# Optimization experiments

Hardware: AMD Instinct MI355X
Metric: run time of the kernel (lower is better)

## Reference

```python
import jax, jax.numpy as jnp
import numpy as np

N = 4608      # total nodes (48 graphs x 96 nodes)
B = 48
NPG = 96
D = 512       # vec_dim
XD = 16       # x_dim
E = N * 32    # GAT edges
L = 6         # GAT layers


def _w(k, shape, fan_in):
    return jax.random.normal(k, shape, jnp.float32) * (1.0 / np.sqrt(fan_in))


def setup_inputs() -> dict:
    key = jax.random.key(0)
    ks = jax.random.split(key, 24)
    x = jax.random.normal(ks[0], (N, XD), jnp.float32)
    xyz = jax.random.normal(ks[1], (N, 3), jnp.float32)
    edge_index = jax.random.randint(ks[2], (2, E), 0, N, dtype=jnp.int32)
    ptr = (jnp.arange(B + 1) * NPG).astype(jnp.int32)
    # complete graph with replacement per segment (torch.combinations order: i<=j)
    i, j = np.triu_indices(NPG)
    offs = (np.arange(B) * NPG)[:, None]
    cloud_edge_index = jnp.asarray(
        np.stack([(i[None, :] + offs).reshape(-1), (j[None, :] + offs).reshape(-1)]),
        jnp.int32)
    return {
        'x': x, 'edge_index': edge_index, 'ptr': ptr, 'xyz': xyz,
        'cloud_edge_index': cloud_edge_index,
        'x_proj_w': _w(ks[3], (XD, D), XD), 'x_proj_b': jnp.zeros((D,), jnp.float32),
        'gat_wl': _w(ks[4], (L, D, D), D), 'gat_bl': jnp.zeros((L, D), jnp.float32),
        'gat_wr': _w(ks[5], (L, D, D), D), 'gat_br': jnp.zeros((L, D), jnp.float32),
        'gat_att': _w(ks[6], (L, D), D), 'gat_bias': jnp.zeros((L, D), jnp.float32),
        'gat_ln_g': jnp.ones((L - 1, D), jnp.float32), 'gat_ln_b': jnp.zeros((L - 1, D), jnp.float32),
        'cg_xyz_w': _w(ks[7], (3, D), 3),
        'cg_bn_g': jnp.ones((D,), jnp.float32), 'cg_bn_b': jnp.zeros((D,), jnp.float32),
        'cg_lin1_w': _w(ks[8], (D, D), D), 'cg_lin1_b': jnp.zeros((D,), jnp.float32),
        'cg_ln_g': jnp.ones((D,), jnp.float32), 'cg_ln_b': jnp.zeros((D,), jnp.float32),
        'lin_w': _w(ks[9], (D, D), D), 'lin_b': jnp.zeros((D,), jnp.float32),
        'bn_g': jnp.ones((D,), jnp.float32), 'bn_b': jnp.zeros((D,), jnp.float32),
    }


def _batchnorm(t, g, b):
    mu = t.mean(0)
    v = ((t - mu) ** 2).mean(0)
    return (t - mu) / jnp.sqrt(v + 1e-5) * g + b


def _forward(x, edge_index, cloud_edge_index, x_proj_w, x_proj_b, gat_wl, gat_bl,
             gat_wr, gat_br, gat_att, gat_bias, gat_ln_g, gat_ln_b, cg_xyz_w,
             cg_bn_g, cg_bn_b, cg_lin1_w, cg_lin1_b, cg_ln_g, cg_ln_b,
             lin_w, lin_b, bn_g, bn_b, xyz):
    n = x.shape[0]
    h = x @ x_proj_w + x_proj_b  # [N, D]
    # ---- GATv2 stack (heads=1, self-loops added, eval mode: no dropout) ----
    loops = jnp.arange(n, dtype=edge_index.dtype)
    ei = jnp.concatenate([edge_index, jnp.stack([loops, loops])], axis=1)
    src, dst = ei[0], ei[1]
    xg = h
    for l in range(L):
        xl = xg @ gat_wl[l] + gat_bl[l]
        xr = xg @ gat_wr[l] + gat_br[l]
        e = jax.nn.leaky_relu(xl[src] + xr[dst], 0.2) @ gat_att[l]  # [E+N]
        m = jax.ops.segment_max(e, dst, num_segments=n)
        ew = jnp.exp(e - m[dst])
        den = jax.ops.segment_sum(ew, dst, num_segments=n)
        alpha = ew / den[dst]
        out = jax.ops.segment_sum(alpha[:, None] * xl[src], dst, num_segments=n) + gat_bias[l]
        if l < L - 1:
            # PyG LayerNorm, mode='graph', batch=None: normalize over all elements
            mu = out.mean()
            sd = jnp.sqrt(((out - mu) ** 2).mean())
            out = (out - mu) / (sd + 1e-5) * gat_ln_g[l] + gat_ln_b[l]
            out = jax.nn.relu(out)
        xg = out
    # ---- CloudGraph (complete graph gather-compute-scatter) ----
    a, b = cloud_edge_index[0], cloud_edge_index[1]
    rx = h[a] - h[b]          # [Ec, D]
    rz = xyz[a] - xyz[b]      # [Ec, 3]
    sq = (rz ** 2).sum(-1)
    dist = jnp.where(sq > 0, jnp.sqrt(jnp.where(sq > 0, sq, 1.0)), 0.0)
    w = jnp.exp(-dist)[:, None]
    p1 = jax.ops.segment_sum(jax.nn.relu((w * rx) @ cg_lin1_w + cg_lin1_b), a, num_segments=n)
    mu1 = p1.mean(-1, keepdims=True)
    v1 = ((p1 - mu1) ** 2).mean(-1, keepdims=True)
    ln1 = (p1 - mu1) / jnp.sqrt(v1 + 1e-5) * cg_ln_g + cg_ln_b
    p2 = jax.ops.segment_sum(jax.nn.relu(rz @ cg_xyz_w), a, num_segments=n)
    xc = h + ln1 + _batchnorm(p2, cg_bn_g, cg_bn_b)
    # ---- fuse + final norm ----
    return _batchnorm((h + xg + xc) @ lin_w + lin_b, bn_g, bn_b)


def reference(x, edge_index, ptr, xyz, cloud_edge_index, x_proj_w, x_proj_b,
              gat_wl, gat_bl, gat_wr, gat_br, gat_att, gat_bias, gat_ln_g,
              gat_ln_b, cg_xyz_w, cg_bn_g, cg_bn_b, cg_lin1_w, cg_lin1_b,
              cg_ln_g, cg_ln_b, lin_w, lin_b, bn_g, bn_b):
    return _forward(x, edge_index, cloud_edge_index, x_proj_w, x_proj_b, gat_wl,
                    gat_bl, gat_wr, gat_br, gat_att, gat_bias, gat_ln_g,
                    gat_ln_b, cg_xyz_w, cg_bn_g, cg_bn_b, cg_lin1_w, cg_lin1_b,
                    cg_ln_g, cg_ln_b, lin_w, lin_b, bn_g, bn_b, xyz)
```

## Files before the change

### kernel.cpp

```cpp
#include <hip/hip_runtime.h>
#include <hip/hip_bf16.h>

#define NN 4608
#define BG 48
#define NPG 96
#define DD 512
#define XDIM 16
#define EREAL 147456
#define NLAYER 6
#define NK 262144
#define TRIU 4656

typedef __hip_bfloat16 bf16;
typedef short short8 __attribute__((ext_vector_type(8)));
typedef short shortx4 __attribute__((ext_vector_type(4)));
typedef float f32x4 __attribute__((ext_vector_type(4)));
typedef float f32x2 __attribute__((ext_vector_type(2)));

__device__ __forceinline__ float s2f(short s) {
  return __uint_as_float(((unsigned int)(unsigned short)s) << 16);
}
__device__ __forceinline__ short f2bs(float f) {
  bf16 h = __float2bfloat16(f);
  short s;
// ... 38 lines not shown
  bf16* dst = Wt + (size_t)z * NK;
  int c = threadIdx.x & 31;
  int r0 = threadIdx.x >> 5;
  int bx = blockIdx.x * 32, by = blockIdx.y * 32;
#pragma unroll
  for (int i = 0; i < 4; i++) {
    int r = r0 + i * 8;
    tile[r][c] = src[(size_t)(by + r) * 512 + bx + c];
  }
  __syncthreads();
#pragma unroll
  for (int i = 0; i < 4; i++) {
    int r = r0 + i * 8;
    dst[(size_t)(bx + r) * 512 + by + c] = __float2bfloat16(tile[c][r]);
  }
}

__global__ void k_xproj(const float* __restrict__ x, const float* __restrict__ w,
                        const float* __restrict__ b, const int* __restrict__ ei,
                        const float* __restrict__ xyz,
                        bf16* __restrict__ h_bf, int* __restrict__ counts,
                        float* __restrict__ ep) {
  int i = blockIdx.x * blockDim.x + threadIdx.x;
  if (i >= NN * DD) return;
  if (i < EREAL) atomicAdd(&counts[ei[EREAL + i]], 1);
  if (i < NN * NPG) {
    int n = i / NPG, e = i - n * NPG;
    int p = n % NPG;
    if (e < NPG - p) {
      int g = n / NPG;
      int slot = g * TRIU + p * NPG - (p * (p - 1)) / 2 + e;
      int j = n + e;
      float dx = xyz[n * 3] - xyz[j * 3];
      float dy = xyz[n * 3 + 1] - xyz[j * 3 + 1];
      float dz = xyz[n * 3 + 2] - xyz[j * 3 + 2];
      float sq = dx * dx + dy * dy + dz * dz;
      float dist = (sq > 0.f) ? sqrtf(sq) : 0.f;
      float4 v;
      v.x = dx; v.y = dy; v.z = dz; v.w = __expf(-dist);
      *(float4*)&ep[(size_t)slot * 4] = v;
    }
  }
  int n = i >> 9, d = i & 511;
  float acc = b[d];
#pragma unroll
  for (int k = 0; k < XDIM; k++) acc += x[n * XDIM + k] * w[k * DD + d];
  h_bf[i] = __float2bfloat16(acc);
}

__global__ void k_scan(const int* __restrict__ counts, int* offsets, int* cursor) {
  __shared__ int part[256];
  int t = threadIdx.x;
  int base = t * 18;
  int s = 0;
#pragma unroll
  for (int i = 0; i < 18; i++) s += counts[base + i];
  part[t] = s;
  __syncthreads();
  for (int off = 1; off < 256; off <<= 1) {
    int v = part[t];
    int u = (t >= off) ? part[t - off] : 0;
    __syncthreads();
    part[t] = v + u;
    __syncthreads();
  }
  int run = t ? part[t - 1] : 0;
#pragma unroll
  for (int i = 0; i < 18; i++) {
    offsets[base + i] = run;
    cursor[base + i] = run;
    run += counts[base + i];
  }
  if (t == 0) offsets[NN] = EREAL;
}
__global__ void k_scatter(const int* __restrict__ ei, int* cursor, int* ssrc) {
  int e = blockIdx.x * blockDim.x + threadIdx.x;
  if (e < EREAL) {
    int s = ei[e], d = ei[EREAL + e];
    int pos = atomicAdd(&cursor[d], 1);
    ssrc[pos] = s;
  }
}

__global__ __launch_bounds__(256) void k_ln(const bf16* __restrict__ in,
                                            bf16* __restrict__ out,
                                            const float* __restrict__ stats,
                                            const float* __restrict__ g,
                                            const float* __restrict__ b) {
  float s = 0.f, ss = 0.f;
#pragma unroll
  for (int i = 0; i < 16; i++) { s += stats[i]; ss += stats[16 + i]; }
  const float invM = 1.f / ((float)NN * (float)DD);
  float mu = s * invM;
  float var = ss * invM - mu * mu;
  float sd = sqrtf(fmaxf(var, 0.f));
  float inv = 1.f / (sd + 1e-5f);
  int i = blockIdx.x * 256 + threadIdx.x;
  int base = i * 8;
  int d0 = base & 511;
  short8 raw = *(const short8*)&in[base];
  short8 pk;
#pragma unroll
  for (int k = 0; k < 8; k++) {
    float t = fmaxf((s2f(raw[k]) - mu) * inv * g[d0 + k] + b[d0 + k], 0.f);
    pk[k] = f2bs(t);
  }
  *(short8*)&out[base] = pk;
}

__global__ __launch_bounds__(256) void k_gemm(
    const bf16* __restrict__ Abf,
    const bf16* __restrict__ B0, const bf16* __restrict__ B1,
    const float* __restrict__ bias0, const float* __restrict__ bias1,
    float* __restrict__ C0, float* __restrict__ C1,
    bf16* __restrict__ Cb0, bf16* __restrict__ Cb1,
    unsigned char* __restrict__ Cf8_0, unsigned char* __restrict__ Cf8_1,
    float* __restrict__ zptr, int zn,
    float* __restrict__ csum, float* __restrict__ csq, int nzl) {
  if (zptr && blockIdx.x == 0) {
    for (int i = threadIdx.x; i < zn; i += 256) zptr[i] = 0.f;
  }
  __shared__ __align__(16) bf16 As[2][128 * 64];
  __shared__ __align__(16) bf16 Bs[2][64 * 64];
  __shared__ float cs[64], cq[64];
  int cpx = gridDim.x >> 3;
  int wgid = (blockIdx.x & 7) * cpx + (blockIdx.x >> 3);
  int mi = wgid >> nzl;
  int r = wgid & ((1 << nzl) - 1);
  int z = r >> 3;
  int m0 = mi * 128, n0 = (r & 7) * 64;

  const bf16* B = z ? B1 : B0;
  const float* bias = z ? bias1 : bias0;
  float* C = z ? C1 : C0;
  bf16* Cb = z ? Cb1 : Cb0;
  unsigned char* Cf8 = z ? Cf8_1 : Cf8_0;
  int tid = threadIdx.x;
  int lane = tid & 63, wid = tid >> 6;
  int mh = (wid >> 1) * 64, nh = (wid & 1) * 32;
  int l15 = lane & 15, quad = lane >> 4;
  int lr8 = lane >> 3;
  int ls8 = lane & 7;
  int c16l = ls8 ^ (lr8 & 7);
  int swzr = (l15 & 7) * 8;

  if (csum && tid < 64) { cs[tid] = 0.f; cq[tid] = 0.f; }

  const bf16* aSrc = Abf + (size_t)(m0 + wid * 32 + lr8) * 512 + c16l * 8;
  const bf16* bSrc = B   + (size_t)(n0 + wid * 16 + lr8) * 512 + c16l * 8;

#define STAGE(bi, kt) do {                                              \
    gl16(aSrc + (kt) * 64,            &As[bi][(wid * 32     ) * 64]);   \
    gl16(aSrc + (kt) * 64 +  8 * 512, &As[bi][(wid * 32 +  8) * 64]);   \
    gl16(aSrc + (kt) * 64 + 16 * 512, &As[bi][(wid * 32 + 16) * 64]);   \
    gl16(aSrc + (kt) * 64 + 24 * 512, &As[bi][(wid * 32 + 24) * 64]);   \
    gl16(bSrc + (kt) * 64,            &Bs[bi][(wid * 16     ) * 64]);   \
    gl16(bSrc + (kt) * 64 +  8 * 512, &Bs[bi][(wid * 16 +  8) * 64]);   \
  } while (0)

  f32x4 acc[4][2];
#pragma unroll
  for (int mt = 0; mt < 4; mt++)
#pragma unroll
    for (int nt = 0; nt < 2; nt++) acc[mt][nt] = (f32x4)0.f;

  STAGE(0, 0);
  __syncthreads();

#pragma unroll
  for (int kt = 0; kt < 8; kt++) {
    const int cur = kt & 1;
    if (kt < 7) STAGE(cur ^ 1, kt + 1);
    short8 af[2][4], bfr[2][2];
#pragma unroll
    for (int kk = 0; kk < 2; kk++) {
#pragma unroll
      for (int mt = 0; mt < 4; mt++)
        af[kk][mt] = *(const short8*)&As[cur][(mh + mt * 16 + l15) * 64 +
                                             (((kk * 4 + quad) * 8) ^ swzr)];
#pragma unroll
      for (int nt = 0; nt < 2; nt++)
        bfr[kk][nt] = *(const short8*)&Bs[cur][(nh + nt * 16 + l15) * 64 +
                                              (((kk * 4 + quad) * 8) ^ swzr)];
    }
#pragma unroll
    for (int kk = 0; kk < 2; kk++)
#pragma unroll
      for (int mt = 0; mt < 4; mt++)
#pragma unroll
        for (int nt = 0; nt < 2; nt++)
          acc[mt][nt] = __builtin_amdgcn_mfma_f32_16x16x32_bf16(
              bfr[kk][nt], af[kk][mt], acc[mt][nt], 0, 0, 0);
    __syncthreads();
  }
#undef STAGE

  float colS[2][4] = {{0.f,0.f,0.f,0.f},{0.f,0.f,0.f,0.f}};
  float colQ[2][4] = {{0.f,0.f,0.f,0.f},{0.f,0.f,0.f,0.f}};
  float bv[2][4] = {{0.f,0.f,0.f,0.f},{0.f,0.f,0.f,0.f}};
#pragma unroll
  for (int nt = 0; nt < 2; nt++) {
    if (bias) {
      float4 b4 = *(const float4*)&bias[n0 + nh + nt * 16 + quad * 4];
      bv[nt][0] = b4.x; bv[nt][1] = b4.y; bv[nt][2] = b4.z; bv[nt][3] = b4.w;
    }
  }
#pragma unroll
  for (int mt = 0; mt < 4; mt++) {
    int row = m0 + mh + mt * 16 + l15;
#pragma unroll
    for (int nt = 0; nt < 2; nt++) {
      int col0 = n0 + nh + nt * 16 + quad * 4;
      float v[4];
#pragma unroll
      for (int r2 = 0; r2 < 4; r2++) {
        v[r2] = acc[mt][nt][r2] + bv[nt][r2];
        if (csum) { colS[nt][r2] += v[r2]; colQ[nt][r2] += v[r2] * v[r2]; }
      }
      if (C) {
        float4 o; o.x = v[0]; o.y = v[1]; o.z = v[2]; o.w = v[3];
        *(float4*)&C[(size_t)row * 512 + col0] = o;
      }
      if (Cb) {
        shortx4 o;
#pragma unroll
        for (int r2 = 0; r2 < 4; r2++) o[r2] = f2bs(v[r2]);
        *(shortx4*)&Cb[(size_t)row * 512 + col0] = o;
      }
      if (Cf8) {
        unsigned int u = __builtin_amdgcn_cvt_pk_fp8_f32(v[0], v[1], 0, false);
        u = __builtin_amdgcn_cvt_pk_fp8_f32(v[2], v[3], u, true);
        *(unsigned int*)&Cf8[(size_t)row * 512 + col0] = u;
      }
    }
  }
  if (csum) {
#pragma unroll
    for (int nt = 0; nt < 2; nt++)
#pragma unroll
      for (int r2 = 0; r2 < 4; r2++) {
        atomicAdd(&cs[nh + nt * 16 + quad * 4 + r2], colS[nt][r2]);
        atomicAdd(&cq[nh + nt * 16 + quad * 4 + r2], colQ[nt][r2]);
      }
    __syncthreads();
    if (tid < 64) {
      atomicAdd(&csum[n0 + tid], cs[tid]);
      atomicAdd(&csq[n0 + tid], cq[tid]);
    }
  }
}

__global__ __launch_bounds__(256) void k_gat_edge(const unsigned char* __restrict__ xl8,
                                                  const bf16* __restrict__ xr,
                                                  const float* __restrict__ att,
                                                  const float* __restrict__ bias,
                                                  const int* __restrict__ offs,
                                                  const int* __restrict__ ssrc,
                                                  bf16* __restrict__ out,
                                                  float* __restrict__ statsOut) {
  __shared__ float redS[4], redSS[4];
  int wave = (blockIdx.x * blockDim.x + threadIdx.x) >> 6;
  int lane = threadIdx.x & 63;
  int wid = threadIdx.x >> 6;
  if (wave < NN) {
    int n = wave;
    int base = lane * 8;
    float xrv[8], attv[8], acc[8];
    short8 xr8 = *(const short8*)&xr[(size_t)n * 512 + base];
#pragma unroll
    for (int k = 0; k < 8; k++) {
      xrv[k] = s2f(xr8[k]);
      attv[k] = att[base + k];
    }
    float m0, lsum;
    {
      uint2 q = *(const uint2*)&xl8[(size_t)n * 512 + base];
      float xs[8];
      f8x4(q.x, xs);
      f8x4(q.y, xs + 4);
      float sc0 = 0.f;
#pragma unroll
      for (int k = 0; k < 8; k++) {
        acc[k] = xs[k];
        float t = xs[k] + xrv[k];
        t = (t > 0.f) ? t : 0.2f * t;
        sc0 += attv[k] * t;
      }
#pragma unroll
      for (int off = 32; off >= 1; off >>= 1) sc0 += __shfl_xor(sc0, off, 64);
      m0 = sc0;
      lsum = 1.f;
    }
    int e0 = offs[n], e1 = offs[n + 1];
    int e = e0;
    for (; e + 3 < e1; e += 4) {
      int s0 = ssrc[e], s1 = ssrc[e + 1], s2 = ssrc[e + 2], s3 = ssrc[e + 3];
      uint2 q0 = *(const uint2*)&xl8[(size_t)s0 * 512 + base];
      uint2 q1 = *(const uint2*)&xl8[(size_t)s1 * 512 + base];
      uint2 q2 = *(const uint2*)&xl8[(size_t)s2 * 512 + base];
      uint2 q3 = *(const uint2*)&xl8[(size_t)s3 * 512 + base];
      float x0[8], x1[8], x2[8], x3[8];
      f8x4(q0.x, x0); f8x4(q0.y, x0 + 4);
      f8x4(q1.x, x1); f8x4(q1.y, x1 + 4);
      f8x4(q2.x, x2); f8x4(q2.y, x2 + 4);
      f8x4(q3.x, x3); f8x4(q3.y, x3 + 4);
      float c0 = 0.f, c1 = 0.f, c2 = 0.f, c3 = 0.f;
#pragma unroll
      for (int k = 0; k < 8; k++) {
        float t0 = x0[k] + xrv[k]; t0 = (t0 > 0.f) ? t0 : 0.2f * t0; c0 += attv[k] * t0;
        float t1 = x1[k] + xrv[k]; t1 = (t1 > 0.f) ? t1 : 0.2f * t1; c1 += attv[k] * t1;
        float t2 = x2[k] + xrv[k]; t2 = (t2 > 0.f) ? t2 : 0.2f * t2; c2 += attv[k] * t2;
        float t3 = x3[k] + xrv[k]; t3 = (t3 > 0.f) ? t3 : 0.2f * t3; c3 += attv[k] * t3;
      }
#pragma unroll
      for (int off = 32; off >= 1; off >>= 1) {
        c0 += __shfl_xor(c0, off, 64);
        c1 += __shfl_xor(c1, off, 64);
        c2 += __shfl_xor(c2, off, 64);
        c3 += __shfl_xor(c3, off, 64);
      }
      float p0 = __expf(c0 - m0), p1 = __expf(c1 - m0);
      float p2 = __expf(c2 - m0), p3 = __expf(c3 - m0);
      lsum += p0 + p1 + p2 + p3;
#pragma unroll
      for (int k = 0; k < 8; k++)
        acc[k] += p0 * x0[k] + p1 * x1[k] + p2 * x2[k] + p3 * x3[k];
    }
    for (; e < e1; ++e) {
      int s0 = ssrc[e];
      uint2 q = *(const uint2*)&xl8[(size_t)s0 * 512 + base];
      float x0[8];
      f8x4(q.x, x0);
      f8x4(q.y, x0 + 4);
      float sc0 = 0.f;
#pragma unroll
      for (int k = 0; k < 8; k++) {
        float t0 = x0[k] + xrv[k];
        t0 = (t0 > 0.f) ? t0 : 0.2f * t0;
        sc0 += attv[k] * t0;
      }
#pragma unroll
      for (int off = 32; off >= 1; off >>= 1) sc0 += __shfl_xor(sc0, off, 64);
      float p0 = __expf(sc0 - m0);
      lsum += p0;
#pragma unroll
      for (int k = 0; k < 8; k++) acc[k] += p0 * x0[k];
    }
    float inv = 1.f / lsum;
    float o[8];
    float s = 0.f, ss = 0.f;
    short8 o8;
#pragma unroll
    for (int k = 0; k < 8; k++) {
      o[k] = acc[k] * inv + bias[base + k];
      s += o[k];
      ss += o[k] * o[k];
      o8[k] = f2bs(o[k]);
    }
    *(short8*)&out[(size_t)n * 512 + base] = o8;
    if (statsOut) {
#pragma unroll
      for (int off = 32; off >= 1; off >>= 1) {
        s += __shfl_xor(s, off, 64);
        ss += __shfl_xor(ss, off, 64);
      }
      if (lane == 0) { redS[wid] = s; redSS[wid] = ss; }
    }
  }
  if (statsOut) {
    __syncthreads();
    if (threadIdx.x == 0) {
      float a = redS[0] + redS[1] + redS[2] + redS[3];
      float b = redSS[0] + redSS[1] + redSS[2] + redSS[3];
      int slot = blockIdx.x & 15;
      atomicAdd(&statsOut[slot], a);
      atomicAdd(&statsOut[16 + slot], b);
    }
  }
}

__global__ __launch_bounds__(256) void k_cloud(const bf16* __restrict__ g1,
                                               const float* __restrict__ ep,
                                               const float* __restrict__ lin1b,
                                               const float* __restrict__ w3,
                                               float* __restrict__ p1,
                                               float* __restrict__ p2) {
  int w = (blockIdx.x * blockDim.x + threadIdx.x) >> 6;
  int lane = threadIdx.x & 63;
  if (w >= NN) return;
  int qh = w & 1;
  int pi = w >> 1;
  int g = pi / 48, pp = pi % 48;
  int d0 = qh * 256 + lane * 4;
  float4 bb4 = *(const float4*)&lin1b[d0];
  float4 w04 = *(const float4*)&w3[d0];
  float4 w14 = *(const float4*)&w3[512 + d0];
  float4 w24 = *(const float4*)&w3[1024 + d0];
  float bb[4] = {bb4.x, bb4.y, bb4.z, bb4.w};
  float w0[4] = {w04.x, w04.y, w04.z, w04.w};
  float w1[4] = {w14.x, w14.y, w14.z, w14.w};
  float w2[4] = {w24.x, w24.y, w24.z, w24.w};

#pragma unroll
  for (int half = 0; half < 2; half++) {
    int p = half ? (NPG - 1 - pp) : pp;
    int n = g * NPG + p;
    int cnt = NPG - p;
    int slot0 = g * TRIU + p * NPG - (p * (p - 1)) / 2;
    const bf16* grow = &g1[(size_t)n * 512 + d0];
    float gi[4];
    { uint2 q = *(const uint2*)grow; bf4(q, gi); }
    float a1[4] = {0.f,0.f,0.f,0.f}, a2[4] = {0.f,0.f,0.f,0.f};
    float b1[4] = {0.f,0.f,0.f,0.f}, b2[4] = {0.f,0.f,0.f,0.f};
    int e = 0;
    for (; e + 3 < cnt; e += 4) {
      int sb = __builtin_amdgcn_readfirstlane(slot0 + e);
      float4 pa = *(const float4*)&ep[(size_t)sb * 4];
      float4 pb = *(const float4*)&ep[(size_t)(sb + 1) * 4];
      float4 pc = *(const float4*)&ep[(size_t)(sb + 2) * 4];
      float4 pd = *(const float4*)&ep[(size_t)(sb + 3) * 4];
      uint2 qa = *(const uint2*)&grow[(size_t)e * 512];
      uint2 qb = *(const uint2*)&grow[(size_t)(e + 1) * 512];
      uint2 qc = *(const uint2*)&grow[(size_t)(e + 2) * 512];
      uint2 qd = *(const uint2*)&grow[(size_t)(e + 3) * 512];
      float xa[4], xb[4], xc[4], xd[4];
      bf4(qa, xa); bf4(qb, xb); bf4(qc, xc); bf4(qd, xd);
      float t;
#pragma unroll
      for (int k = 0; k < 4; k++) {
        t = fmaf(pa.w, gi[k] - xa[k], bb[k]); a1[k] += fmaxf(t, 0.f);
        t = fmaf(pb.w, gi[k] - xb[k], bb[k]); b1[k] += fmaxf(t, 0.f);
        t = fmaf(pc.w, gi[k] - xc[k], bb[k]); a1[k] += fmaxf(t, 0.f);
        t = fmaf(pd.w, gi[k] - xd[k], bb[k]); b1[k] += fmaxf(t, 0.f);
        t = pa.x * w0[k] + pa.y * w1[k] + pa.z * w2[k]; a2[k] += fmaxf(t, 0.f);
        t = pb.x * w0[k] + pb.y * w1[k] + pb.z * w2[k]; b2[k] += fmaxf(t, 0.f);
        t = pc.x * w0[k] + pc.y * w1[k] + pc.z * w2[k]; a2[k] += fmaxf(t, 0.f);
        t = pd.x * w0[k] + pd.y * w1[k] + pd.z * w2[k]; b2[k] += fmaxf(t, 0.f);
      }
    }
    for (; e < cnt; ++e) {
      float4 pa = *(const float4*)&ep[(size_t)(slot0 + e) * 4];
      uint2 qa = *(const uint2*)&grow[(size_t)e * 512];
      float xa[4];
      bf4(qa, xa);
      float t;
#pragma unroll
      for (int k = 0; k < 4; k++) {
        t = fmaf(pa.w, gi[k] - xa[k], bb[k]); a1[k] += fmaxf(t, 0.f);
        t = pa.x * w0[k] + pa.y * w1[k] + pa.z * w2[k]; a2[k] += fmaxf(t, 0.f);
      }
    }
    float4 o1, o2;
    o1.x = a1[0] + b1[0]; o1.y = a1[1] + b1[1];
    o1.z = a1[2] + b1[2]; o1.w = a1[3] + b1[3];
    o2.x = a2[0] + b2[0]; o2.y = a2[1] + b2[1];
    o2.z = a2[2] + b2[2]; o2.w = a2[3] + b2[3];
    *(float4*)&p1[(size_t)n * 512 + d0] = o1;
    *(float4*)&p2[(size_t)n * 512 + d0] = o2;
  }
}

__global__ __launch_bounds__(256) void k_cloud_epi(
    const float* __restrict__ p1, const float* __restrict__ p2,
    const bf16* __restrict__ h_bf, const bf16* __restrict__ xg_bf,
    const float* __restrict__ colsum, const float* __restrict__ colsq,
    const float* __restrict__ lng, const float* __restrict__ lnb,
    const float* __restrict__ bng, const float* __restrict__ bnb,
    bf16* __restrict__ s_bf, float* __restrict__ zptr) {
  if (blockIdx.x == 0) {
    for (int i = threadIdx.x; i < 1024; i += 256) zptr[i] = 0.f;
  }
  int wave = (blockIdx.x * blockDim.x + threadIdx.x) >> 6;
  int lane = threadIdx.x & 63;
  if (wave >= NN) return;
  int n = wave;
  size_t rb = (size_t)n * 512 + lane * 8;
  int base = lane * 8;
  float v[8];
  float s = 0.f;
#pragma unroll
  for (int k = 0; k < 8; k++) {
    v[k] = p1[rb + k];
    s += v[k];
  }
#pragma unroll
  for (int off = 32; off >= 1; off >>= 1) s += __shfl_xor(s, off, 64);
  float mu = s * (1.f / 512.f);
  float ss = 0.f;
#pragma unroll
  for (int k = 0; k < 8; k++) {
    float t = v[k] - mu;
    ss += t * t;
  }
#pragma unroll
  for (int off = 32; off >= 1; off >>= 1) ss += __shfl_xor(ss, off, 64);
  float inv = 1.f / sqrtf(ss * (1.f / 512.f) + 1e-5f);
  short8 hb = *(const short8*)&h_bf[rb];
  short8 xb = *(const short8*)&xg_bf[rb];
  short8 o8;
#pragma unroll
  for (int k = 0; k < 8; k++) {
    int d = base + k;
    float ln1 = (v[k] - mu) * inv * lng[d] + lnb[d];
    float cmu = colsum[d] * (1.f / NN);
    float cvar = colsq[d] * (1.f / NN) - cmu * cmu;
    float cinv = 1.f / sqrtf(fmaxf(cvar, 0.f) + 1e-5f);
    float bnv = (p2[rb + k] - cmu) * cinv * bng[d] + bnb[d];
    float out = 2.f * s2f(hb[k]) + s2f(xb[k]) + ln1 + bnv;
    o8[k] = f2bs(out);
  }
  *(short8*)&s_bf[rb] = o8;
}

__global__ void k_col_reduce(const float* __restrict__ x, float* colsum, float* colsq) {
  int r0 = blockIdx.x * 32;
  int c0 = threadIdx.x;
  float s0 = 0.f, q0 = 0.f, s1 = 0.f, q1 = 0.f;
  for (int r = r0; r < r0 + 32; ++r) {
    float v = x[(size_t)r * 512 + c0];
    s0 += v;
    q0 += v * v;
    float w = x[(size_t)r * 512 + c0 + 256];
    s1 += w;
    q1 += w * w;
  }
  atomicAdd(&colsum[c0], s0);
  atomicAdd(&colsq[c0], q0);
  atomicAdd(&colsum[c0 + 256], s1);
  atomicAdd(&colsq[c0 + 256], q1);
}
__global__ void k_bn_out(const float* __restrict__ y, const float* __restrict__ colsum,
                         const float* __restrict__ colsq, const float* __restrict__ g,
                         const float* __restrict__ b, float* __restrict__ out) {
  int i = blockIdx.x * blockDim.x + threadIdx.x;
  if (i >= NN * DD) return;
  int d = i & 511;
  float mu = colsum[d] * (1.f / NN);
  float var = colsq[d] * (1.f / NN) - mu * mu;
  float inv = 1.f / sqrtf(fmaxf(var, 0.f) + 1e-5f);
  out[i] = (y[i] - mu) * inv * g[d] + b[d];
}

extern "C" void kernel_launch(void* const* d_in, const int* in_sizes, int n_in,
                              void* d_out, int out_size, void* d_ws, size_t ws_size,
                              hipStream_t stream) {
  const float* x = (const float*)d_in[0];
  const int* ei = (const int*)d_in[1];
  const float* xyz = (const float*)d_in[3];
  const float* x_proj_w = (const float*)d_in[5];
  const float* x_proj_b = (const float*)d_in[6];
  const float* gat_wl = (const float*)d_in[7];
  const float* gat_bl = (const float*)d_in[8];
  const float* gat_wr = (const float*)d_in[9];
  const float* gat_br = (const float*)d_in[10];
  const float* gat_att = (const float*)d_in[11];
  const float* gat_bias = (const float*)d_in[12];
  const float* gat_ln_g = (const float*)d_in[13];
  const float* gat_ln_b = (const float*)d_in[14];
  const float* cg_xyz_w = (const float*)d_in[15];
  const float* cg_bn_g = (const float*)d_in[16];
  const float* cg_bn_b = (const float*)d_in[17];
  const float* cg_lin1_w = (const float*)d_in[18];
  const float* cg_lin1_b = (const float*)d_in[19];
  const float* cg_ln_g = (const float*)d_in[20];
  const float* cg_ln_b = (const float*)d_in[21];
  const float* lin_w = (const float*)d_in[22];
  const float* lin_b = (const float*)d_in[23];
  const float* bn_g = (const float*)d_in[24];
  const float* bn_b = (const float*)d_in[25];

  const size_t ND = (size_t)NN * DD;
  char* w = (char*)d_ws;
  float* p1 = (float*)w;       w += ND * 4;
  float* p2 = (float*)w;       w += ND * 4;
  bf16* h_bf = (bf16*)w;       w += ND * 2;
  bf16* xg_bf = (bf16*)w;      w += ND * 2;
  bf16* g1_bf = (bf16*)w;      w += ND * 2;
  bf16* xr_bf = (bf16*)w;      w += ND * 2;
  unsigned char* xl_f8 = (unsigned char*)w; w += ND;
  bf16* Wt = (bf16*)w;         w += (size_t)14 * NK * 2;
  float* eparam = (float*)w;   w += (size_t)BG * TRIU * 16;
  int* counts = (int*)w;       w += NN * 4;
  int* offs = (int*)w;         w += (NN + 4) * 4;
  int* cursor = (int*)w;       w += NN * 4;
  int* ssrc = (int*)w;         w += EREAL * 4;
  float* statsAll = (float*)w; w += 5 * 32 * 4;
  float* colsum = (float*)w;   w += 512 * 4;
  float* colsq = (float*)w;    w += 512 * 4;
  float* colsum2 = (float*)w;  w += 512 * 4;
  float* colsq2 = (float*)w;   w += 512 * 4;
  float* y = p1;
  bf16* s_bf = h_bf;
  bf16* aln_bf = g1_bf;

  const int TPB = 256;
  const int ND_BLK = (int)((ND + TPB - 1) / TPB);

  k_wt<<<dim3(16, 16, 14), TPB, 0, stream>>>(gat_wl, gat_wr, cg_lin1_w, lin_w, Wt,
                                             counts, statsAll);
  k_xproj<<<ND_BLK, TPB, 0, stream>>>(x, x_proj_w, x_proj_b, ei, xyz, h_bf,
                                      counts, eparam);
  k_scan<<<1, 256, 0, stream>>>(counts, offs, cursor);
  k_scatter<<<(EREAL + TPB - 1) / TPB, TPB, 0, stream>>>(ei, cursor, ssrc);

  for (int l = 0; l < NLAYER; l++) {
    const bf16* A;
    if (l == 0) {
      A = h_bf;
    } else {
      k_ln<<<(int)(ND / 8 / TPB), TPB, 0, stream>>>(
          xg_bf, aln_bf, statsAll + 32 * (l - 1),
          gat_ln_g + (size_t)(l - 1) * DD, gat_ln_b + (size_t)(l - 1) * DD);
      A = aln_bf;
    }
    k_gemm<<<576, TPB, 0, stream>>>(
        A, Wt + (size_t)l * NK, Wt + (size_t)(6 + l) * NK,
        gat_bl + l * DD, gat_br + l * DD, nullptr, nullptr, nullptr, xr_bf,
        xl_f8, nullptr, nullptr, 0, nullptr, nullptr, 4);
    float* sOut = (l < NLAYER - 1) ? statsAll + 32 * l : nullptr;
    k_gat_edge<<<NN / 4, TPB, 0, stream>>>(xl_f8, xr_bf, gat_att + l * DD,
                                           gat_bias + l * DD, offs, ssrc,
                                           xg_bf, sOut);
  }

  k_gemm<<<288, TPB, 0, stream>>>(
      h_bf, Wt + (size_t)12 * NK, Wt + (size_t)12 * NK, nullptr, nullptr,
      nullptr, nullptr, g1_bf, g1_bf, nullptr, nullptr,
      colsum, 1024, nullptr, nullptr, 3);
  k_cloud<<<NN / 4, TPB, 0, stream>>>(g1_bf, eparam, cg_lin1_b, cg_xyz_w, p1, p2);
  k_col_reduce<<<144, 256, 0, stream>>>(p2, colsum, colsq);
  k_cloud_epi<<<NN / 4, TPB, 0, stream>>>(p1, p2, h_bf, xg_bf, colsum, colsq,
                                          cg_ln_g, cg_ln_b, cg_bn_g, cg_bn_b,
                                          s_bf, colsum2);

  k_gemm<<<288, TPB, 0, stream>>>(
      s_bf, Wt + (size_t)13 * NK, Wt + (size_t)13 * NK, lin_b, lin_b,
      y, y, nullptr, nullptr, nullptr, nullptr,
      nullptr, 0, colsum2, colsq2, 3);
  k_bn_out<<<ND_BLK, TPB, 0, stream>>>(y, colsum2, colsq2, bn_g, bn_b,
                                       (float*)d_out);
}
```

Baseline: 542.6 us.

## Merge cloud-branch kernels into GAT layer launches to fill the GPU

The cloud lin1 GEMM becomes extra blocks of the layer-0 GAT projection GEMM. The cloud pairwise aggregation becomes extra blocks of the layer-0 edge kernel, split into half-waves per node pair. The p2 column reduction runs as extra blocks of the layer-1 LayerNorm kernel, which now also writes in place into xg. This removes three launches and lets the independent cloud branch fill idle CUs during small GAT kernels, at the cost of heterogeneous blocks and possible load imbalance.

Result: faster. 522.7 us (-3.7%).

```diff
diff --git a/kernel.cpp b/kernel.cpp
--- a/kernel.cpp
+++ b/kernel.cpp
@@ -144,11 +144,29 @@
   }
 }
 
-__global__ __launch_bounds__(256) void k_ln(const bf16* __restrict__ in,
-                                            bf16* __restrict__ out,
+__global__ __launch_bounds__(256) void k_ln(bf16* __restrict__ xg,
                                             const float* __restrict__ stats,
                                             const float* __restrict__ g,
-                                            const float* __restrict__ b) {
+                                            const float* __restrict__ b,
+                                            const float* __restrict__ p2,
+                                            float* __restrict__ colsum,
+                                            float* __restrict__ colsq) {
+  if ((int)blockIdx.x >= 1152) {
+    int r0 = (blockIdx.x - 1152) * 32;
+    int c0 = threadIdx.x;
+    float s0 = 0.f, q0 = 0.f, s1 = 0.f, q1 = 0.f;
+    for (int r = r0; r < r0 + 32; ++r) {
+      float v = p2[(size_t)r * 512 + c0];
+      s0 += v; q0 += v * v;
+      float w = p2[(size_t)r * 512 + c0 + 256];
+      s1 += w; q1 += w * w;
+    }
+    atomicAdd(&colsum[c0], s0);
+    atomicAdd(&colsq[c0], q0);
+    atomicAdd(&colsum[c0 + 256], s1);
+    atomicAdd(&colsq[c0 + 256], q1);
+    return;
+  }
   float s = 0.f, ss = 0.f;
 #pragma unroll
   for (int i = 0; i < 16; i++) { s += stats[i]; ss += stats[16 + i]; }
@@ -160,30 +178,146 @@
   int i = blockIdx.x * 256 + threadIdx.x;
   int base = i * 8;
   int d0 = base & 511;
-  short8 raw = *(const short8*)&in[base];
+  short8 raw = *(const short8*)&xg[base];
   short8 pk;
 #pragma unroll
   for (int k = 0; k < 8; k++) {
     float t = fmaxf((s2f(raw[k]) - mu) * inv * g[d0 + k] + b[d0 + k], 0.f);
     pk[k] = f2bs(t);
   }
-  *(short8*)&out[base] = pk;
+  *(short8*)&xg[base] = pk;
+}
+
+__device__ __forceinline__ void gemm_tile(
+    const bf16* __restrict__ Abf, const bf16* __restrict__ B,
+    const float* __restrict__ bias,
+    float* __restrict__ C, bf16* __restrict__ Cb, unsigned char* __restrict__ Cf8,
+    float* __restrict__ csum, float* __restrict__ csq,
+    int m0, int n0, bf16* As, bf16* Bs, float* cs, float* cq) {
+  int tid = threadIdx.x;
+  int lane = tid & 63, wid = tid >> 6;
+  int mh = (wid >> 1) * 64, nh = (wid & 1) * 32;
+  int l15 = lane & 15, quad = lane >> 4;
+  int lr8 = lane >> 3, ls8 = lane & 7;
+  int c16l = ls8 ^ lr8;
+  int swzr = (l15 & 7) * 8;
+
+  if (csum && tid < 64) { cs[tid] = 0.f; cq[tid] = 0.f; }
+
+  const bf16* aSrc = Abf + (size_t)(m0 + wid * 32 + lr8) * 512 + c16l * 8;
+  const bf16* bSrc = B   + (size_t)(n0 + wid * 16 + lr8) * 512 + c16l * 8;
+
+#define STAGE(bi, kt) do {                                                   \
+    gl16(aSrc + (kt) * 64,            As + (bi) * 8192 + (wid * 32     ) * 64); \
+    gl16(aSrc + (kt) * 64 +  8 * 512, As + (bi) * 8192 + (wid * 32 +  8) * 64); \
+    gl16(aSrc + (kt) * 64 + 16 * 512, As + (bi) * 8192 + (wid * 32 + 16) * 64); \
+    gl16(aSrc + (kt) * 64 + 24 * 512, As + (bi) * 8192 + (wid * 32 + 24) * 64); \
+    gl16(bSrc + (kt) * 64,            Bs + (bi) * 4096 + (wid * 16     ) * 64); \
+    gl16(bSrc + (kt) * 64 +  8 * 512, Bs + (bi) * 4096 + (wid * 16 +  8) * 64); \
+  } while (0)
+
+  f32x4 acc[4][2];
+#pragma unroll
+  for (int mt = 0; mt < 4; mt++)
+#pragma unroll
+    for (int nt = 0; nt < 2; nt++) acc[mt][nt] = (f32x4)0.f;
+
+  STAGE(0, 0);
+  __syncthreads();
+
+#pragma unroll
+  for (int kt = 0; kt < 8; kt++) {
+    const int cur = kt & 1;
+    if (kt < 7) STAGE(cur ^ 1, kt + 1);
+    short8 af[2][4], bfr[2][2];
+#pragma unroll
+    for (int kk = 0; kk < 2; kk++) {
+#pragma unroll
+      for (int mt = 0; mt < 4; mt++)
+        af[kk][mt] = *(const short8*)&As[cur * 8192 + (mh + mt * 16 + l15) * 64 +
+                                        (((kk * 4 + quad) * 8) ^ swzr)];
+#pragma unroll
+      for (int nt = 0; nt < 2; nt++)
+        bfr[kk][nt] = *(const short8*)&Bs[cur * 4096 + (nh + nt * 16 + l15) * 64 +
+                                         (((kk * 4 + quad) * 8) ^ swzr)];
+    }
+#pragma unroll
+    for (int kk = 0; kk < 2; kk++)
+#pragma unroll
+      for (int mt = 0; mt < 4; mt++)
+#pragma unroll
+        for (int nt = 0; nt < 2; nt++)
+          acc[mt][nt] = __builtin_amdgcn_mfma_f32_16x16x32_bf16(
+              bfr[kk][nt], af[kk][mt], acc[mt][nt], 0, 0, 0);
+    __syncthreads();
+  }
+#undef STAGE
+
+  float colS[2][4] = {{0.f,0.f,0.f,0.f},{0.f,0.f,0.f,0.f}};
+  float colQ[2][4] = {{0.f,0.f,0.f,0.f},{0.f,0.f,0.f,0.f}};
+  float bv[2][4] = {{0.f,0.f,0.f,0.f},{0.f,0.f,0.f,0.f}};
+#pragma unroll
+  for (int nt = 0; nt < 2; nt++) {
+    if (bias) {
+      float4 b4 = *(const float4*)&bias[n0 + nh + nt * 16 + quad * 4];
+      bv[nt][0] = b4.x; bv[nt][1] = b4.y; bv[nt][2] = b4.z; bv[nt][3] = b4.w;
+    }
+  }
+#pragma unroll
+  for (int mt = 0; mt < 4; mt++) {
+    int row = m0 + mh + mt * 16 + l15;
+#pragma unroll
+    for (int nt = 0; nt < 2; nt++) {
+      int col0 = n0 + nh + nt * 16 + quad * 4;
+      float v[4];
+#pragma unroll
+      for (int r2 = 0; r2 < 4; r2++) {
+        v[r2] = acc[mt][nt][r2] + bv[nt][r2];
+        if (csum) { colS[nt][r2] += v[r2]; colQ[nt][r2] += v[r2] * v[r2]; }
+      }
+      if (C) {
+        float4 o; o.x = v[0]; o.y = v[1]; o.z = v[2]; o.w = v[3];
+        *(float4*)&C[(size_t)row * 512 + col0] = o;
+      }
+      if (Cb) {
+        shortx4 o;
+#pragma unroll
+        for (int r2 = 0; r2 < 4; r2++) o[r2] = f2bs(v[r2]);
+        *(shortx4*)&Cb[(size_t)row * 512 + col0] = o;
+      }
+      if (Cf8) {
+        unsigned int u = __builtin_amdgcn_cvt_pk_fp8_f32(v[0], v[1], 0, false);
+        u = __builtin_amdgcn_cvt_pk_fp8_f32(v[2], v[3], u, true);
+        *(unsigned int*)&Cf8[(size_t)row * 512 + col0] = u;
+      }
+    }
+  }
+  if (csum) {
+#pragma unroll
+    for (int nt = 0; nt < 2; nt++)
+#pragma unroll
+      for (int r2 = 0; r2 < 4; r2++) {
+        atomicAdd(&cs[nh + nt * 16 + quad * 4 + r2], colS[nt][r2]);
+        atomicAdd(&cq[nh + nt * 16 + quad * 4 + r2], colQ[nt][r2]);
+      }
+    __syncthreads();
+    if (tid < 64) {
+      atomicAdd(&csum[n0 + tid], cs[tid]);
+      atomicAdd(&csq[n0 + tid], cq[tid]);
+    }
+  }
 }
 
 __global__ __launch_bounds__(256) void k_gemm(
     const bf16* __restrict__ Abf,
     const bf16* __restrict__ B0, const bf16* __restrict__ B1,
     const float* __restrict__ bias0, const float* __restrict__ bias1,
-    float* __restrict__ C0, float* __restrict__ C1,
+    float* __restrict__ C0,
     bf16* __restrict__ Cb0, bf16* __restrict__ Cb1,
-    unsigned char* __restrict__ Cf8_0, unsigned char* __restrict__ Cf8_1,
-    float* __restrict__ zptr, int zn,
+    unsigned char* __restrict__ Cf8_0,
     float* __restrict__ csum, float* __restrict__ csq, int nzl) {
-  if (zptr && blockIdx.x == 0) {
-    for (int i = threadIdx.x; i < zn; i += 256) zptr[i] = 0.f;
-  }
-  __shared__ __align__(16) bf16 As[2][128 * 64];
-  __shared__ __align__(16) bf16 Bs[2][64 * 64];
+  __shared__ __align__(16) bf16 As[2 * 128 * 64];
+  __shared__ __align__(16) bf16 Bs[2 * 64 * 64];
   __shared__ float cs[64], cq[64];
   int cpx = gridDim.x >> 3;
   int wgid = (blockIdx.x & 7) * cpx + (blockIdx.x >> 3);
@@ -191,136 +325,52 @@
   int r = wgid & ((1 << nzl) - 1);
   int z = r >> 3;
   int m0 = mi * 128, n0 = (r & 7) * 64;
-
-  const bf16* B = z ? B1 : B0;
-  const float* bias = z ? bias1 : bias0;
-  float* C = z ? C1 : C0;
-  bf16* Cb = z ? Cb1 : Cb0;
-  unsigned char* Cf8 = z ? Cf8_1 : Cf8_0;
-  int tid = threadIdx.x;
-  int lane = tid & 63, wid = tid >> 6;
-  int mh = (wid >> 1) * 64, nh = (wid & 1) * 32;
-  int l15 = lane & 15, quad = lane >> 4;
-  int lr8 = lane >> 3;
-  int ls8 = lane & 7;
-  int c16l = ls8 ^ (lr8 & 7);
-  int swzr = (l15 & 7) * 8;
-
-  if (csum && tid < 64) { cs[tid] = 0.f; cq[tid] = 0.f; }
-
-  const bf16* aSrc = Abf + (size_t)(m0 + wid * 32 + lr8) * 512 + c16l * 8;
-  const bf16* bSrc = B   + (size_t)(n0 + wid * 16 + lr8) * 512 + c16l * 8;
-
-#define STAGE(bi, kt) do {                                              \
-    gl16(aSrc + (kt) * 64,            &As[bi][(wid * 32     ) * 64]);   \
-    gl16(aSrc + (kt) * 64 +  8 * 512, &As[bi][(wid * 32 +  8) * 64]);   \
-    gl16(aSrc + (kt) * 64 + 16 * 512, &As[bi][(wid * 32 + 16) * 64]);   \
-    gl16(aSrc + (kt) * 64 + 24 * 512, &As[bi][(wid * 32 + 24) * 64]);   \
-    gl16(bSrc + (kt) * 64,            &Bs[bi][(wid * 16     ) * 64]);   \
-    gl16(bSrc + (kt) * 64 +  8 * 512, &Bs[bi][(wid * 16 +  8) * 64]);   \
-  } while (0)
-
-  f32x4 acc[4][2];
-#pragma unroll
-  for (int mt = 0; mt < 4; mt++)
-#pragma unroll
-    for (int nt = 0; nt < 2; nt++) acc[mt][nt] = (f32x4)0.f;
-
-  STAGE(0, 0);
-  __syncthreads();
-
-#pragma unroll
-  for (int kt = 0; kt < 8; kt++) {
-    const int cur = kt & 1;
-    if (kt < 7) STAGE(cur ^ 1, kt + 1);
-    short8 af[2][4], bfr[2][2];
-#pragma unroll
-    for (int kk = 0; kk < 2; kk++) {
-#pragma unroll
-      for (int mt = 0; mt < 4; mt++)
-        af[kk][mt] = *(const short8*)&As[cur][(mh + mt * 16 + l15) * 64 +
-                                             (((kk * 4 + quad) * 8) ^ swzr)];
-#pragma unroll
-      for (int nt = 0; nt < 2; nt++)
-        bfr[kk][nt] = *(const short8*)&Bs[cur][(nh + nt * 16 + l15) * 64 +
-                                              (((kk * 4 + quad) * 8) ^ swzr)];
-    }
-#pragma unroll
-    for (int kk = 0; kk < 2; kk++)
-#pragma unroll
-      for (int mt = 0; mt < 4; mt++)
-#pragma unroll
-        for (int nt = 0; nt < 2; nt++)
-          acc[mt][nt] = __builtin_amdgcn_mfma_f32_16x16x32_bf16(
-              bfr[kk][nt], af[kk][mt], acc[mt][nt], 0, 0, 0);
-    __syncthreads();
-  }
-#undef STAGE
-
-  float colS[2][4] = {{0.f,0.f,0.f,0.f},{0.f,0.f,0.f,0.f}};
-  float colQ[2][4] = {{0.f,0.f,0.f,0.f},{0.f,0.f,0.f,0.f}};
-  float bv[2][4] = {{0.f,0.f,0.f,0.f},{0.f,0.f,0.f,0.f}};
-#pragma unroll
-  for (int nt = 0; nt < 2; nt++) {
-    if (bias) {
-      float4 b4 = *(const float4*)&bias[n0 + nh + nt * 16 + quad * 4];
-      bv[nt][0] = b4.x; bv[nt][1] = b4.y; bv[nt][2] = b4.z; bv[nt][3] = b4.w;
-    }
-  }
-#pragma unroll
-  for (int mt = 0; mt < 4; mt++) {
-    int row = m0 + mh + mt * 16 + l15;
-#pragma unroll
-    for (int nt = 0; nt < 2; nt++) {
-      int col0 = n0 + nh + nt * 16 + quad * 4;
-      float v[4];
-#pragma unroll
-      for (int r2 = 0; r2 < 4; r2++) {
-        v[r2] = acc[mt][nt][r2] + bv[nt][r2];
-        if (csum) { colS[nt][r2] += v[r2]; colQ[nt][r2] += v[r2] * v[r2]; }
-      }
-      if (C) {
-        float4 o; o.x = v[0]; o.y = v[1]; o.z = v[2]; o.w = v[3];
-        *(float4*)&C[(size_t)row * 512 + col0] = o;
-      }
-      if (Cb) {
-        shortx4 o;
-#pragma unroll
-        for (int r2 = 0; r2 < 4; r2++) o[r2] = f2bs(v[r2]);
-        *(shortx4*)&Cb[(size_t)row * 512 + col0] = o;
-      }
-      if (Cf8) {
-        unsigned int u = __builtin_amdgcn_cvt_pk_fp8_f32(v[0], v[1], 0, false);
-        u = __builtin_amdgcn_cvt_pk_fp8_f32(v[2], v[3], u, true);
-        *(unsigned int*)&Cf8[(size_t)row * 512 + col0] = u;
-      }
-    }
-  }
-  if (csum) {
-#pragma unroll
-    for (int nt = 0; nt < 2; nt++)
-#pragma unroll
-      for (int r2 = 0; r2 < 4; r2++) {
-        atomicAdd(&cs[nh + nt * 16 + quad * 4 + r2], colS[nt][r2]);
-        atomicAdd(&cq[nh + nt * 16 + quad * 4 + r2], colQ[nt][r2]);
-      }
-    __syncthreads();
-    if (tid < 64) {
-      atomicAdd(&csum[n0 + tid], cs[tid]);
-      atomicAdd(&csq[n0 + tid], cq[tid]);
-    }
-  }
-}
-
-__global__ __launch_bounds__(256) void k_gat_edge(const unsigned char* __restrict__ xl8,
-                                                  const bf16* __restrict__ xr,
-                                                  const float* __restrict__ att,
-                                                  const float* __restrict__ bias,
-                                                  const int* __restrict__ offs,
-                                                  const int* __restrict__ ssrc,
-                                                  bf16* __restrict__ out,
-                                                  float* __restrict__ statsOut) {
-  __shared__ float redS[4], redSS[4];
+  gemm_tile(Abf, z ? B1 : B0, z ? bias1 : bias0,
+            z ? nullptr : C0, z ? Cb1 : Cb0, z ? nullptr : Cf8_0,
+            csum, csq, m0, n0, As, Bs, cs, cq);
+}
+
+__global__ __launch_bounds__(256) void k_gemm_l0(
+    const bf16* __restrict__ h_bf,
+    const bf16* __restrict__ Bl, const bf16* __restrict__ Br,
+    const float* __restrict__ biasl, const float* __restrict__ biasr,
+    bf16* __restrict__ xr_bf, unsigned char* __restrict__ xl_f8,
+    const bf16* __restrict__ Bg1, bf16* __restrict__ g1_bf,
+    float* __restrict__ zptr) {
+  __shared__ __align__(16) bf16 As[2 * 128 * 64];
+  __shared__ __align__(16) bf16 Bs[2 * 64 * 64];
+  int b = blockIdx.x;
+  if (b < 576) {
+    int cpx = 576 >> 3;
+    int wgid = (b & 7) * cpx + (b >> 3);
+    int mi = wgid >> 4;
+    int r = wgid & 15;
+    int z = r >> 3;
+    int m0 = mi * 128, n0 = (r & 7) * 64;
+    gemm_tile(h_bf, z ? Br : Bl, z ? biasr : biasl,
+              nullptr, z ? xr_bf : nullptr, z ? nullptr : xl_f8,
+              nullptr, nullptr, m0, n0, As, Bs, nullptr, nullptr);
+  } else {
+    int b2 = b - 576;
+    if (b2 == 0) {
+      for (int i = threadIdx.x; i < 1024; i += 256) zptr[i] = 0.f;
+    }
+    int cpx = 288 >> 3;
+    int wgid = (b2 & 7) * cpx + (b2 >> 3);
+    int mi = wgid >> 3;
+    int r = wgid & 7;
+    int m0 = mi * 128, n0 = r * 64;
+    gemm_tile(h_bf, Bg1, nullptr, nullptr, g1_bf, nullptr,
+              nullptr, nullptr, m0, n0, As, Bs, nullptr, nullptr);
+  }
+}
+
+__device__ __forceinline__ void edge_block(
+    const unsigned char* __restrict__ xl8, const bf16* __restrict__ xr,
+    const float* __restrict__ att, const float* __restrict__ bias,
+    const int* __restrict__ offs, const int* __restrict__ ssrc,
+    bf16* __restrict__ out, float* __restrict__ statsOut,
+    float* redS, float* redSS) {
   int wave = (blockIdx.x * blockDim.x + threadIdx.x) >> 6;
   int lane = threadIdx.x & 63;
   int wid = threadIdx.x >> 6;
@@ -441,18 +491,15 @@
   }
 }
 
-__global__ __launch_bounds__(256) void k_cloud(const bf16* __restrict__ g1,
-                                               const float* __restrict__ ep,
-                                               const float* __restrict__ lin1b,
-                                               const float* __restrict__ w3,
-                                               float* __restrict__ p1,
-                                               float* __restrict__ p2) {
-  int w = (blockIdx.x * blockDim.x + threadIdx.x) >> 6;
-  int lane = threadIdx.x & 63;
-  if (w >= NN) return;
+__device__ __forceinline__ void cloud_wave(
+    const bf16* __restrict__ g1, const float* __restrict__ ep,
+    const float* __restrict__ lin1b, const float* __restrict__ w3,
+    float* __restrict__ p1, float* __restrict__ p2, int w, int lane) {
   int qh = w & 1;
-  int pi = w >> 1;
+  int half = (w >> 1) & 1;
+  int pi = w >> 2;
   int g = pi / 48, pp = pi % 48;
+  int p = half ? (NPG - 1 - pp) : pp;
   int d0 = qh * 256 + lane * 4;
   float4 bb4 = *(const float4*)&lin1b[d0];
   float4 w04 = *(const float4*)&w3[d0];
@@ -463,62 +510,84 @@
   float w1[4] = {w14.x, w14.y, w14.z, w14.w};
   float w2[4] = {w24.x, w24.y, w24.z, w24.w};
 
-#pragma unroll
-  for (int half = 0; half < 2; half++) {
-    int p = half ? (NPG - 1 - pp) : pp;
-    int n = g * NPG + p;
-    int cnt = NPG - p;
-    int slot0 = g * TRIU + p * NPG - (p * (p - 1)) / 2;
-    const bf16* grow = &g1[(size_t)n * 512 + d0];
-    float gi[4];
-    { uint2 q = *(const uint2*)grow; bf4(q, gi); }
-    float a1[4] = {0.f,0.f,0.f,0.f}, a2[4] = {0.f,0.f,0.f,0.f};
-    float b1[4] = {0.f,0.f,0.f,0.f}, b2[4] = {0.f,0.f,0.f,0.f};
-    int e = 0;
-    for (; e + 3 < cnt; e += 4) {
-      int sb = __builtin_amdgcn_readfirstlane(slot0 + e);
-      float4 pa = *(const float4*)&ep[(size_t)sb * 4];
-      float4 pb = *(const float4*)&ep[(size_t)(sb + 1) * 4];
-      float4 pc = *(const float4*)&ep[(size_t)(sb + 2) * 4];
-      float4 pd = *(const float4*)&ep[(size_t)(sb + 3) * 4];
-      uint2 qa = *(const uint2*)&grow[(size_t)e * 512];
-      uint2 qb = *(const uint2*)&grow[(size_t)(e + 1) * 512];
-      uint2 qc = *(const uint2*)&grow[(size_t)(e + 2) * 512];
-      uint2 qd = *(const uint2*)&grow[(size_t)(e + 3) * 512];
-      float xa[4], xb[4], xc[4], xd[4];
-      bf4(qa, xa); bf4(qb, xb); bf4(qc, xc); bf4(qd, xd);
-      float t;
-#pragma unroll
-      for (int k = 0; k < 4; k++) {
-        t = fmaf(pa.w, gi[k] - xa[k], bb[k]); a1[k] += fmaxf(t, 0.f);
-        t = fmaf(pb.w, gi[k] - xb[k], bb[k]); b1[k] += fmaxf(t, 0.f);
-        t = fmaf(pc.w, gi[k] - xc[k], bb[k]); a1[k] += fmaxf(t, 0.f);
-        t = fmaf(pd.w, gi[k] - xd[k], bb[k]); b1[k] += fmaxf(t, 0.f);
-        t = pa.x * w0[k] + pa.y * w1[k] + pa.z * w2[k]; a2[k] += fmaxf(t, 0.f);
-        t = pb.x * w0[k] + pb.y * w1[k] + pb.z * w2[k]; b2[k] += fmaxf(t, 0.f);
-        t = pc.x * w0[k] + pc.y * w1[k] + pc.z * w2[k]; a2[k] += fmaxf(t, 0.f);
-        t = pd.x * w0[k] + pd.y * w1[k] + pd.z * w2[k]; b2[k] += fmaxf(t, 0.f);
-      }
-    }
-    for (; e < cnt; ++e) {
-      float4 pa = *(const float4*)&ep[(size_t)(slot0 + e) * 4];
-      uint2 qa = *(const uint2*)&grow[(size_t)e * 512];
-      float xa[4];
-      bf4(qa, xa);
-      float t;
-#pragma unroll
-      for (int k = 0; k < 4; k++) {
-        t = fmaf(pa.w, gi[k] - xa[k], bb[k]); a1[k] += fmaxf(t, 0.f);
-        t = pa.x * w0[k] + pa.y * w1[k] + pa.z * w2[k]; a2[k] += fmaxf(t, 0.f);
-      }
-    }
-    float4 o1, o2;
-    o1.x = a1[0] + b1[0]; o1.y = a1[1] + b1[1];
-    o1.z = a1[2] + b1[2]; o1.w = a1[3] + b1[3];
-    o2.x = a2[0] + b2[0]; o2.y = a2[1] + b2[1];
-    o2.z = a2[2] + b2[2]; o2.w = a2[3] + b2[3];
-    *(float4*)&p1[(size_t)n * 512 + d0] = o1;
-    *(float4*)&p2[(size_t)n * 512 + d0] = o2;
+  int n = g * NPG + p;
+  int cnt = NPG - p;
+  int slot0 = g * TRIU + p * NPG - (p * (p - 1)) / 2;
+  const bf16* grow = &g1[(size_t)n * 512 + d0];
+  float gi[4];
+  { uint2 q = *(const uint2*)grow; bf4(q, gi); }
+  float a1[4] = {0.f,0.f,0.f,0.f}, a2[4] = {0.f,0.f,0.f,0.f};
+  float b1[4] = {0.f,0.f,0.f,0.f}, b2[4] = {0.f,0.f,0.f,0.f};
+  int e = 0;
+  for (; e + 3 < cnt; e += 4) {
+    int sb = __builtin_amdgcn_readfirstlane(slot0 + e);
+    float4 pa = *(const float4*)&ep[(size_t)sb * 4];
+    float4 pb = *(const float4*)&ep[(size_t)(sb + 1) * 4];
+    float4 pc = *(const float4*)&ep[(size_t)(sb + 2) * 4];
+    float4 pd = *(const float4*)&ep[(size_t)(sb + 3) * 4];
+    uint2 qa = *(const uint2*)&grow[(size_t)e * 512];
+    uint2 qb = *(const uint2*)&grow[(size_t)(e + 1) * 512];
+    uint2 qc = *(const uint2*)&grow[(size_t)(e + 2) * 512];
+    uint2 qd = *(const uint2*)&grow[(size_t)(e + 3) * 512];
+    float xa[4], xb[4], xc[4], xd[4];
+    bf4(qa, xa); bf4(qb, xb); bf4(qc, xc); bf4(qd, xd);
+    float t;
+#pragma unroll
+    for (int k = 0; k < 4; k++) {
+      t = fmaf(pa.w, gi[k] - xa[k], bb[k]); a1[k] += fmaxf(t, 0.f);
+      t = fmaf(pb.w, gi[k] - xb[k], bb[k]); b1[k] += fmaxf(t, 0.f);
+      t = fmaf(pc.w, gi[k] - xc[k], bb[k]); a1[k] += fmaxf(t, 0.f);
+      t = fmaf(pd.w, gi[k] - xd[k], bb[k]); b1[k] += fmaxf(t, 0.f);
+      t = pa.x * w0[k] + pa.y * w1[k] + pa.z * w2[k]; a2[k] += fmaxf(t, 0.f);
+      t = pb.x * w0[k] + pb.y * w1[k] + pb.z * w2[k]; b2[k] += fmaxf(t, 0.f);
+      t = pc.x * w0[k] + pc.y * w1[k] + pc.z * w2[k]; a2[k] += fmaxf(t, 0.f);
+      t = pd.x * w0[k] + pd.y * w1[k] + pd.z * w2[k]; b2[k] += fmaxf(t, 0.f);
+    }
+  }
+  for (; e < cnt; ++e) {
+    float4 pa = *(const float4*)&ep[(size_t)(slot0 + e) * 4];
+    uint2 qa = *(const uint2*)&grow[(size_t)e * 512];
+    float xa[4];
+    bf4(qa, xa);
+    float t;
+#pragma unroll
+    for (int k = 0; k < 4; k++) {
+      t = fmaf(pa.w, gi[k] - xa[k], bb[k]); a1[k] += fmaxf(t, 0.f);
+      t = pa.x * w0[k] + pa.y * w1[k] + pa.z * w2[k]; a2[k] += fmaxf(t, 0.f);
+    }
+  }
+  float4 o1, o2;
+  o1.x = a1[0] + b1[0]; o1.y = a1[1] + b1[1];
+  o1.z = a1[2] + b1[2]; o1.w = a1[3] + b1[3];
+  o2.x = a2[0] + b2[0]; o2.y = a2[1] + b2[1];
+  o2.z = a2[2] + b2[2]; o2.w = a2[3] + b2[3];
+  *(float4*)&p1[(size_t)n * 512 + d0] = o1;
+  *(float4*)&p2[(size_t)n * 512 + d0] = o2;
+}
+
+__global__ __launch_bounds__(256) void k_gat_edge(
+    const unsigned char* __restrict__ xl8, const bf16* __restrict__ xr,
+    const float* __restrict__ att, const float* __restrict__ bias,
+    const int* __restrict__ offs, const int* __restrict__ ssrc,
+    bf16* __restrict__ out, float* __restrict__ statsOut) {
+  __shared__ float redS[4], redSS[4];
+  edge_block(xl8, xr, att, bias, offs, ssrc, out, statsOut, redS, redSS);
+}
+
+__global__ __launch_bounds__(256) void k_edge_cloud(
+    const unsigned char* __restrict__ xl8, const bf16* __restrict__ xr,
+    const float* __restrict__ att, const float* __restrict__ bias,
+    const int* __restrict__ offs, const int* __restrict__ ssrc,
+    bf16* __restrict__ out, float* __restrict__ statsOut,
+    const bf16* __restrict__ g1, const float* __restrict__ ep,
+    const float* __restrict__ lin1b, const float* __restrict__ w3,
+    float* __restrict__ p1, float* __restrict__ p2) {
+  __shared__ float redS[4], redSS[4];
+  if ((int)blockIdx.x < 1152) {
+    edge_block(xl8, xr, att, bias, offs, ssrc, out, statsOut, redS, redSS);
+  } else {
+    int w = (blockIdx.x - 1152) * 4 + (threadIdx.x >> 6);
+    cloud_wave(g1, ep, lin1b, w3, p1, p2, w, threadIdx.x & 63);
   }
 }
 
@@ -574,23 +643,6 @@
   *(short8*)&s_bf[rb] = o8;
 }
 
-__global__ void k_col_reduce(const float* __restrict__ x, float* colsum, float* colsq) {
-  int r0 = blockIdx.x * 32;
-  int c0 = threadIdx.x;
-  float s0 = 0.f, q0 = 0.f, s1 = 0.f, q1 = 0.f;
-  for (int r = r0; r < r0 + 32; ++r) {
-    float v = x[(size_t)r * 512 + c0];
-    s0 += v;
-    q0 += v * v;
-    float w = x[(size_t)r * 512 + c0 + 256];
-    s1 += w;
-    q1 += w * w;
-  }
-  atomicAdd(&colsum[c0], s0);
-  atomicAdd(&colsq[c0], q0);
-  atomicAdd(&colsum[c0 + 256], s1);
-  atomicAdd(&colsq[c0 + 256], q1);
-}
 __global__ void k_bn_out(const float* __restrict__ y, const float* __restrict__ colsum,
                          const float* __restrict__ colsq, const float* __restrict__ g,
                          const float* __restrict__ b, float* __restrict__ out) {
@@ -653,7 +705,6 @@
   float* colsq2 = (float*)w;   w += 512 * 4;
   float* y = p1;
   bf16* s_bf = h_bf;
-  bf16* aln_bf = g1_bf;
 
   const int TPB = 256;
   const int ND_BLK = (int)((ND + TPB - 1) / TPB);
@@ -665,40 +716,35 @@
   k_scan<<<1, 256, 0, stream>>>(counts, offs, cursor);
   k_scatter<<<(EREAL + TPB - 1) / TPB, TPB, 0, stream>>>(ei, cursor, ssrc);
 
-  for (int l = 0; l < NLAYER; l++) {
-    const bf16* A;
-    if (l == 0) {
-      A = h_bf;
-    } else {
-      k_ln<<<(int)(ND / 8 / TPB), TPB, 0, stream>>>(
-          xg_bf, aln_bf, statsAll + 32 * (l - 1),
-          gat_ln_g + (size_t)(l - 1) * DD, gat_ln_b + (size_t)(l - 1) * DD);
-      A = aln_bf;
-    }
+  k_gemm_l0<<<864, TPB, 0, stream>>>(h_bf, Wt, Wt + (size_t)6 * NK,
+                                     gat_bl, gat_br, xr_bf, xl_f8,
+                                     Wt + (size_t)12 * NK, g1_bf, colsum);
+  k_edge_cloud<<<1152 + 2304, TPB, 0, stream>>>(
+      xl_f8, xr_bf, gat_att, gat_bias, offs, ssrc, xg_bf, statsAll,
+      g1_bf, eparam, cg_lin1_b, cg_xyz_w, p1, p2);
+
+  for (int l = 1; l < NLAYER; l++) {
+    k_ln<<<(l == 1) ? 1296 : 1152, TPB, 0, stream>>>(
+        xg_bf, statsAll + 32 * (l - 1),
+        gat_ln_g + (size_t)(l - 1) * DD, gat_ln_b + (size_t)(l - 1) * DD,
+        (l == 1) ? p2 : nullptr, colsum, colsq);
     k_gemm<<<576, TPB, 0, stream>>>(
-        A, Wt + (size_t)l * NK, Wt + (size_t)(6 + l) * NK,
-        gat_bl + l * DD, gat_br + l * DD, nullptr, nullptr, nullptr, xr_bf,
-        xl_f8, nullptr, nullptr, 0, nullptr, nullptr, 4);
+        xg_bf, Wt + (size_t)l * NK, Wt + (size_t)(6 + l) * NK,
+        gat_bl + l * DD, gat_br + l * DD, nullptr, nullptr, xr_bf,
+        xl_f8, nullptr, nullptr, 4);
     float* sOut = (l < NLAYER - 1) ? statsAll + 32 * l : nullptr;
     k_gat_edge<<<NN / 4, TPB, 0, stream>>>(xl_f8, xr_bf, gat_att + l * DD,
                                            gat_bias + l * DD, offs, ssrc,
                                            xg_bf, sOut);
   }
 
-  k_gemm<<<288, TPB, 0, stream>>>(
-      h_bf, Wt + (size_t)12 * NK, Wt + (size_t)12 * NK, nullptr, nullptr,
-      nullptr, nullptr, g1_bf, g1_bf, nullptr, nullptr,
-      colsum, 1024, nullptr, nullptr, 3);
-  k_cloud<<<NN / 4, TPB, 0, stream>>>(g1_bf, eparam, cg_lin1_b, cg_xyz_w, p1, p2);
-  k_col_reduce<<<144, 256, 0, stream>>>(p2, colsum, colsq);
   k_cloud_epi<<<NN / 4, TPB, 0, stream>>>(p1, p2, h_bf, xg_bf, colsum, colsq,
                                           cg_ln_g, cg_ln_b, cg_bn_g, cg_bn_b,
                                           s_bf, colsum2);
 
   k_gemm<<<288, TPB, 0, stream>>>(
       s_bf, Wt + (size_t)13 * NK, Wt + (size_t)13 * NK, lin_b, lin_b,
-      y, y, nullptr, nullptr, nullptr, nullptr,
-      nullptr, 0, colsum2, colsq2, 3);
+      y, nullptr, nullptr, nullptr, colsum2, colsq2, 3);
   k_bn_out<<<ND_BLK, TPB, 0, stream>>>(y, colsum2, colsq2, bn_g, bn_b,
                                        (float*)d_out);
 }
```
